# Optimization experiments

Measured on AMD Instinct MI355X. Metric: run time of the kernel, lower is better.

The kernel has to match this reference:

```python
import jax, jax.numpy as jnp
import numpy as np

B, L, E, H = 8, 4096, 1024, 16
D = E // H


def setup_inputs() -> dict:
    key = jax.random.key(0)
    ks = jax.random.split(key, 9)
    s = 1.0 / np.sqrt(E)
    inp = {"x": jax.random.normal(ks[0], (B, L, E), dtype=jnp.float32)}
    names = ["Wq", "bq", "Wk", "bk", "Wv", "bv", "Wo", "bo"]
    for i, n in enumerate(names):
        if n.startswith("W"):
            inp[n] = jax.random.uniform(ks[i + 1], (E, E), dtype=jnp.float32, minval=-s, maxval=s)
        else:
            inp[n] = jax.random.uniform(ks[i + 1], (E,), dtype=jnp.float32, minval=-s, maxval=s)
    return inp


def reference(x, Wq, bq, Wk, bk, Wv, bv, Wo, bo):
    Bb, Ll, _ = x.shape
    # projections: weight is (out, in), y = x @ W^T + b
    Q = jnp.einsum('bli,oi->blo', x, Wq) + bq
    K = jnp.einsum('bli,oi->blo', x, Wk) + bk
    V = jnp.einsum('bli,oi->blo', x, Wv) + bv
    # [B, H, L, D]
    Q = Q.reshape(Bb, Ll, H, D).transpose(0, 2, 1, 3)
    K = K.reshape(Bb, Ll, H, D).transpose(0, 2, 1, 3)
    V = V.reshape(Bb, Ll, H, D).transpose(0, 2, 1, 3)
    # auto-correlation along sequence axis (axis=2)
    q_fft = jnp.fft.rfft(Q, axis=2)
    k_fft = jnp.fft.rfft(K, axis=2)
    corr_time = jnp.fft.irfft(q_fft * jnp.conjugate(k_fft), n=Ll, axis=2)
    corr = jnp.mean(corr_time, axis=-1)              # [B, H, L]
    attn = jax.nn.softmax(corr, axis=-1)             # [B, H, L]
    out = jnp.einsum('bhl,bhld->bhd', attn, V)       # [B, H, D]
    out = out.transpose(0, 2, 1).reshape(Bb, E)      # [B, E] (D-major interleave, as in source)
    out = jnp.einsum('bi,oi->bo', out, Wo) + bo      # [B, E]
    return jnp.repeat(out[:, None, :], Ll, axis=1)   # [B, L, E]
```

## Files before the change

kernel.cpp:

```cpp
#include <hip/hip_runtime.h>
#include <hip/hip_bf16.h>
#include <math.h>

#define B_ 8
#define L_ 4096
#define E_ 1024
#define H_ 16
#define D_ 64

typedef short short8 __attribute__((ext_vector_type(8)));
typedef float f32x4 __attribute__((ext_vector_type(4)));

__device__ __forceinline__ unsigned short f2bf(float f) {
  unsigned int u = __float_as_uint(f);
  unsigned int r = u + 0x7FFFu + ((u >> 16) & 1u);
  return (unsigned short)(r >> 16);
}
__device__ __forceinline__ float bf2f(unsigned short h) {
  return __uint_as_float(((unsigned int)h) << 16);
}

#define GLDS16(g, l)                                                     \
  __builtin_amdgcn_global_load_lds(                                      \
      (const __attribute__((address_space(1))) void*)(g),                \
      (__attribute__((address_space(3))) void*)(l), 16, 0, 0)

__global__ __launch_bounds__(256) void conv_w(
    const float* __restrict__ Wq, const float* __restrict__ Wk,
    const float* __restrict__ Wv, unsigned short* __restrict__ Wb) {
  const int wsel = blockIdx.y;
  const float* W = (wsel == 0) ? Wq : (wsel == 1) ? Wk : Wv;
  size_t i = ((size_t)blockIdx.x * 256 + threadIdx.x) * 4;
  float4 f = *(const float4*)(W + i);
  size_t o = (size_t)wsel * (1024 * 1024) + i;
  *(ushort4*)(Wb + o) =
      make_ushort4(f2bf(f.x), f2bf(f.y), f2bf(f.z), f2bf(f.w));
}

__global__ __launch_bounds__(256) void conv_x(const float* __restrict__ x,
                                              unsigned short* __restrict__ xb) {
  const size_t total = (size_t)B_ * L_ * E_ / 8;
  for (size_t i = (size_t)blockIdx.x * blockDim.x + threadIdx.x; i < total;
       i += (size_t)gridDim.x * blockDim.x) {
    float4 a = ((const float4*)x)[i * 2];
    float4 b = ((const float4*)x)[i * 2 + 1];
    short8 v;
    v[0] = (short)f2bf(a.x); v[1] = (short)f2bf(a.y);
    v[2] = (short)f2bf(a.z); v[3] = (short)f2bf(a.w);
    v[4] = (short)f2bf(b.x); v[5] = (short)f2bf(b.y);
    v[6] = (short)f2bf(b.z); v[7] = (short)f2bf(b.w);
    *(short8*)&xb[i * 8] = v;
  }
}

#define STAGE_A(buf, h, s, t)                                                \
  GLDS16(xb + (size_t)(m0 + (s)*128 + (h)*64 + srow) * E_ + (t)*64 + scol,   \
         &sA[buf][((s)*128 + (h)*64 + wid * 8) * 64])
#define STAGE_B(buf, h, s, t)                                                \
  GLDS16(Wb + (size_t)(n0 + (s)*128 + (h)*32 + brow_i) * E_ + (t)*64 + scol, \
         &sB[buf][((s)*128 + (h)*32 + bw) * 64])

__global__ __launch_bounds__(512) void qkv_gemm8(
    const unsigned short* __restrict__ xb,
    const unsigned short* __restrict__ Wb, const float* __restrict__ bq,
    const float* __restrict__ bk, const float* __restrict__ bv,
    unsigned short* __restrict__ QTb, unsigned short* __restrict__ KTb,
    unsigned short* __restrict__ Vb) {
  __shared__ unsigned short sA[2][256 * 64];
  __shared__ unsigned short sB[2][256 * 64];

  const int tid = threadIdx.x;
  const int wid = tid >> 6, lane = tid & 63;
  const int wr = wid >> 2, wc = wid & 3;
  const int fr = lane & 15, fg = lane >> 4, fr7 = fr & 7;
  const int n0 = blockIdx.x * 256;
  const int m0 = blockIdx.y * 256;

  const int srow = tid >> 3;
  const int scol = ((tid & 7) ^ (srow & 7)) * 8;
  const int brow_i = ((srow >> 5) << 6) + (srow & 31);
  const int bw = ((wid >> 2) << 6) + ((wid & 3) << 3);

  f32x4 acc[8][4];
#pragma unroll
  for (int i = 0; i < 8; ++i)
#pragma unroll
    for (int j = 0; j < 4; ++j) acc[i][j] = (f32x4){0.f, 0.f, 0.f, 0.f};

  STAGE_A(0, 0, 0, 0); STAGE_A(0, 0, 1, 0);
  STAGE_A(0, 1, 0, 0); STAGE_A(0, 1, 1, 0);
  STAGE_B(0, 0, 0, 0); STAGE_B(0, 0, 1, 0);
  STAGE_B(0, 1, 0, 0); STAGE_B(0, 1, 1, 0);
  STAGE_A(1, 0, 0, 1); STAGE_A(1, 0, 1, 1);
  STAGE_B(1, 0, 0, 1); STAGE_B(1, 0, 1, 1);

  const int NT = E_ / 64;
  for (int u = 0; u < NT; ++u) {
    const int cur = u & 1, nxt = cur ^ 1;
    __builtin_amdgcn_sched_barrier(0);
    if (u == NT - 1)
      asm volatile("s_waitcnt vmcnt(0)" ::: "memory");
    else
      asm volatile("s_waitcnt vmcnt(4)" ::: "memory");
    __builtin_amdgcn_sched_barrier(0);
    __builtin_amdgcn_s_barrier();

    short8 af[4][2], b0[2][2], b1[2][2];
#pragma unroll
    for (int i = 0; i < 4; ++i)
#pragma unroll
      for (int kk = 0; kk < 2; ++kk) {
        const int blk = (((kk * 4 + fg) ^ fr7) << 3);
        af[i][kk] = *(const short8*)
            &sA[cur][(wr * 128 + i * 16 + fr) * 64 + blk];
      }
#pragma unroll
    for (int j = 0; j < 2; ++j)
#pragma unroll
      for (int kk = 0; kk < 2; ++kk) {
        const int blk = (((kk * 4 + fg) ^ fr7) << 3);
        b0[j][kk] = *(const short8*)
            &sB[cur][(wc * 64 + j * 16 + fr) * 64 + blk];
        b1[j][kk] = *(const short8*)
            &sB[cur][(wc * 64 + (2 + j) * 16 + fr) * 64 + blk];
      }
    if (u + 1 < NT) {
      STAGE_A(nxt, 1, 0, u + 1); STAGE_A(nxt, 1, 1, u + 1);
      STAGE_B(nxt, 1, 0, u + 1); STAGE_B(nxt, 1, 1, u + 1);
    }
    asm volatile("s_waitcnt lgkmcnt(0)" ::: "memory");
    __builtin_amdgcn_sched_barrier(0);
    __builtin_amdgcn_s_setprio(1);
#pragma unroll
    for (int i = 0; i < 4; ++i)
#pragma unroll
      for (int kk = 0; kk < 2; ++kk) {
        acc[i][0] = __builtin_amdgcn_mfma_f32_16x16x32_bf16(af[i][kk], b0[0][kk], acc[i][0], 0, 0, 0);
        acc[i][1] = __builtin_amdgcn_mfma_f32_16x16x32_bf16(af[i][kk], b0[1][kk], acc[i][1], 0, 0, 0);
        acc[i][2] = __builtin_amdgcn_mfma_f32_16x16x32_bf16(af[i][kk], b1[0][kk], acc[i][2], 0, 0, 0);
        acc[i][3] = __builtin_amdgcn_mfma_f32_16x16x32_bf16(af[i][kk], b1[1][kk], acc[i][3], 0, 0, 0);
      }
    __builtin_amdgcn_s_setprio(0);
    __builtin_amdgcn_s_barrier();

#pragma unroll
    for (int i = 0; i < 4; ++i)
#pragma unroll
      for (int kk = 0; kk < 2; ++kk) {
        const int blk = (((kk * 4 + fg) ^ fr7) << 3);
        af[i][kk] = *(const short8*)
            &sA[cur][(wr * 128 + 64 + i * 16 + fr) * 64 + blk];
      }
    if (u + 2 < NT) {
      STAGE_A(cur, 0, 0, u + 2); STAGE_A(cur, 0, 1, u + 2);
      STAGE_B(cur, 0, 0, u + 2); STAGE_B(cur, 0, 1, u + 2);
    }
    asm volatile("s_waitcnt lgkmcnt(0)" ::: "memory");
    __builtin_amdgcn_sched_barrier(0);
    __builtin_amdgcn_s_setprio(1);
#pragma unroll
    for (int i = 0; i < 4; ++i)
#pragma unroll
      for (int kk = 0; kk < 2; ++kk) {
        acc[4 + i][0] = __builtin_amdgcn_mfma_f32_16x16x32_bf16(af[i][kk], b0[0][kk], acc[4 + i][0], 0, 0, 0);
        acc[4 + i][1] = __builtin_amdgcn_mfma_f32_16x16x32_bf16(af[i][kk], b0[1][kk], acc[4 + i][1], 0, 0, 0);
        acc[4 + i][2] = __builtin_amdgcn_mfma_f32_16x16x32_bf16(af[i][kk], b1[0][kk], acc[4 + i][2], 0, 0, 0);
        acc[4 + i][3] = __builtin_amdgcn_mfma_f32_16x16x32_bf16(af[i][kk], b1[1][kk], acc[4 + i][3], 0, 0, 0);
      }
    __builtin_amdgcn_s_setprio(0);
  }

  const int wsel = n0 >> 10;
  const float* bias = (wsel == 0) ? bq : (wsel == 1) ? bk : bv;
  float br[4];
#pragma unroll
  for (int j = 0; j < 4; ++j)
    br[j] = bias[(n0 & 1023) + wc * 64 + j * 16 + fr];

  if (wsel < 2) {
    unsigned short* T = (wsel == 0) ? QTb : KTb;
    const int b = m0 >> 12;
    const int lbase = (m0 & 4095) + wr * 128 + (fg << 2);
#pragma unroll
    for (int i = 0; i < 8; ++i)
#pragma unroll
      for (int j = 0; j < 4; ++j) {
        const int n_in = (n0 & 1023) + wc * 64 + j * 16 + fr;
        ushort4 v = make_ushort4(f2bf(acc[i][j][0] + br[j]),
                                 f2bf(acc[i][j][1] + br[j]),
                                 f2bf(acc[i][j][2] + br[j]),
                                 f2bf(acc[i][j][3] + br[j]));
        *(ushort4*)&T[((size_t)(b << 10) + n_in) * L_ + lbase + i * 16] = v;
      }
  } else {
#pragma unroll
    for (int i = 0; i < 8; ++i)
#pragma unroll
      for (int j = 0; j < 4; ++j) {
        const int n_in = (n0 & 1023) + wc * 64 + j * 16 + fr;
#pragma unroll
        for (int r = 0; r < 4; ++r) {
          const int m = m0 + wr * 128 + i * 16 + (fg << 2) + r;
          Vb[(size_t)m * E_ + n_in] = f2bf(acc[i][j][r] + br[j]);
        }
      }
  }
}

__device__ __forceinline__ float2 cmulf(float2 a, float2 b) {
  return make_float2(a.x * b.x - a.y * b.y, a.x * b.y + a.y * b.x);
}

__device__ __forceinline__ float2 herm(float2 Zf, float2 Zc) {
  float ax = Zc.x, ay = -Zc.y;
  float qx = 0.5f * (Zf.x + ax), qy = 0.5f * (Zf.y + ay);
  float ux = Zf.x - ax, uy = Zf.y - ay;
  float kx = 0.5f * uy, ky = -0.5f * ux;
  return make_float2(qx * kx + qy * ky, qy * kx - qx * ky);
}

__global__ __launch_bounds__(512) void corr_fft(
    const unsigned short* __restrict__ QTb,
    const unsigned short* __restrict__ KTb, float2* __restrict__ Spart) {
  __shared__ float2 bufA[L_];
  __shared__ float2 bufB[L_];

  const int bh = blockIdx.x, ds = blockIdx.y;
  const int b = bh >> 4, h = bh & (H_ - 1);
  const int tid = threadIdx.x;
  const float sign = -1.0f;

  float2 tw[6], tw5b;
  {
    const float TWO_PI = 6.28318530717958647692f;
#pragma unroll
    for (int st = 0; st < 6; ++st) {
      const int Ns = 1 << (2 * st);
      const int r = tid & (Ns - 1);
      float ang = sign * TWO_PI * (float)r / (float)(4 * Ns);
      __sincosf(ang, &tw[st].y, &tw[st].x);
    }
    const int r5 = (tid + 512) & 1023;
    float ang = sign * TWO_PI * (float)r5 / 4096.f;
    __sincosf(ang, &tw5b.y, &tw5b.x);
  }

  float2 s[4];
#pragma unroll
  for (int q = 0; q < 4; ++q) s[q] = make_float2(0.f, 0.f);

  const size_t baseQK = (size_t)(b * E_ + h * D_) * L_;

  for (int dd = 0; dd < 8; ++dd) {
    const int d = ds * 8 + dd;
    __syncthreads();
    const unsigned short* qp = QTb + baseQK + (size_t)d * L_;
    const unsigned short* kp = KTb + baseQK + (size_t)d * L_;
    {
      ushort4 qa = *(const ushort4*)(qp + tid * 8);
      ushort4 qb = *(const ushort4*)(qp + tid * 8 + 4);
      ushort4 ka = *(const ushort4*)(kp + tid * 8);
      ushort4 kb = *(const ushort4*)(kp + tid * 8 + 4);
      bufA[tid * 8 + 0] = make_float2(bf2f(qa.x), bf2f(ka.x));
      bufA[tid * 8 + 1] = make_float2(bf2f(qa.y), bf2f(ka.y));
      bufA[tid * 8 + 2] = make_float2(bf2f(qa.z), bf2f(ka.z));
      bufA[tid * 8 + 3] = make_float2(bf2f(qa.w), bf2f(ka.w));
      bufA[tid * 8 + 4] = make_float2(bf2f(qb.x), bf2f(kb.x));
      bufA[tid * 8 + 5] = make_float2(bf2f(qb.y), bf2f(kb.y));
      bufA[tid * 8 + 6] = make_float2(bf2f(qb.z), bf2f(kb.z));
      bufA[tid * 8 + 7] = make_float2(bf2f(qb.w), bf2f(kb.w));
    }
    float2* cur = bufA;
    float2* nxt = bufB;
#pragma unroll
    for (int st = 0; st < 6; ++st) {
      const int Ns = 1 << (2 * st);
      __syncthreads();
#pragma unroll
      for (int h2 = 0; h2 < 2; ++h2) {
        const int j = tid + h2 * 512;
        float2 v0 = cur[j];
        float2 v1 = cur[j + 1024];
        float2 v2 = cur[j + 2048];
        float2 v3 = cur[j + 3072];
        const int r = j & (Ns - 1);
        if (st > 0) {
          float2 w1 = (st == 5 && h2 == 1) ? tw5b : tw[st];
          float2 w2 = cmulf(w1, w1);
          float2 w3 = cmulf(w2, w1);
          v1 = cmulf(v1, w1);
          v2 = cmulf(v2, w2);
          v3 = cmulf(v3, w3);
        }
        float2 t0 = make_float2(v0.x + v2.x, v0.y + v2.y);
        float2 t1 = make_float2(v0.x - v2.x, v0.y - v2.y);
        float2 t2 = make_float2(v1.x + v3.x, v1.y + v3.y);
        float2 t3 = make_float2(v1.x - v3.x, v1.y - v3.y);
        float2 t3i = make_float2(-sign * t3.y, sign * t3.x);
        const int idxD = ((j - r) << 2) + r;
        nxt[idxD]          = make_float2(t0.x + t2.x, t0.y + t2.y);
        nxt[idxD + Ns]     = make_float2(t1.x + t3i.x, t1.y + t3i.y);
        nxt[idxD + 2 * Ns] = make_float2(t0.x - t2.x, t0.y - t2.y);
        nxt[idxD + 3 * Ns] = make_float2(t1.x - t3i.x, t1.y - t3i.y);
      }
      float2* tmp = cur; cur = nxt; nxt = tmp;
    }
    __syncthreads();
#pragma unroll
    for (int q = 0; q < 4; ++q) {
      const int f = tid + q * 512;
      float2 Zf = bufA[f];
      float2 Zc = bufA[(L_ - f) & (L_ - 1)];
      float2 r = herm(Zf, Zc);
      s[q].x += r.x;
      s[q].y += r.y;
    }
    if (tid == 0) {
      float2 Zf = bufA[2048];
      float2 r = herm(Zf, Zf);
      s[0].y += r.x;
    }
  }
  float2* out = Spart + (size_t)(bh * 8 + ds) * (L_ / 2);
#pragma unroll
  for (int q = 0; q < 4; ++q) out[tid + q * 512] = s[q];
}

__device__ __forceinline__ void fft_tw_init(float2* tw, int tid, float sign) {
  const float TWO_PI = 6.28318530717958647692f;
#pragma unroll
  for (int st = 0; st < 6; ++st) {
    const int Ns = 1 << (2 * st);
    const int r = tid & (Ns - 1);
    float ang = sign * TWO_PI * (float)r / (float)(4 * Ns);
    __sincosf(ang, &tw[st].y, &tw[st].x);
  }
}

__device__ __forceinline__ void fft4096_tw(float2* __restrict__ A,
                                           float2* __restrict__ Bb, int tid,
                                           float sign,
                                           const float2* __restrict__ tw) {
  float2* cur = A;
  float2* nxt = Bb;
#pragma unroll
  for (int st = 0; st < 6; ++st) {
    const int Ns = 1 << (2 * st);
    __syncthreads();
    const int j = tid;
    float2 v0 = cur[j];
    float2 v1 = cur[j + 1024];
    float2 v2 = cur[j + 2048];
    float2 v3 = cur[j + 3072];
    const int r = j & (Ns - 1);
    if (st > 0) {
      float2 w1 = tw[st];
      float2 w2 = cmulf(w1, w1);
      float2 w3 = cmulf(w2, w1);
      v1 = cmulf(v1, w1);
      v2 = cmulf(v2, w2);
      v3 = cmulf(v3, w3);
    }
    float2 t0 = make_float2(v0.x + v2.x, v0.y + v2.y);
    float2 t1 = make_float2(v0.x - v2.x, v0.y - v2.y);
    float2 t2 = make_float2(v1.x + v3.x, v1.y + v3.y);
    float2 t3 = make_float2(v1.x - v3.x, v1.y - v3.y);
    float2 t3i = make_float2(-sign * t3.y, sign * t3.x);
    const int idxD = ((j - r) << 2) + r;
    nxt[idxD]          = make_float2(t0.x + t2.x, t0.y + t2.y);
    nxt[idxD + Ns]     = make_float2(t1.x + t3i.x, t1.y + t3i.y);
    nxt[idxD + 2 * Ns] = make_float2(t0.x - t2.x, t0.y - t2.y);
    nxt[idxD + 3 * Ns] = make_float2(t1.x - t3i.x, t1.y - t3i.y);
    float2* tmp = cur; cur = nxt; nxt = tmp;
  }
  __syncthreads();
}

__global__ __launch_bounds__(1024) void corr_post(
    const float2* __restrict__ Spart, float* __restrict__ attnW) {
  __shared__ float2 bufA[L_];
  __shared__ float2 bufB[L_];
  __shared__ float red[1024];

  const int bh = blockIdx.x;
  const int tid = threadIdx.x;

  float2 tw[6];
  fft_tw_init(tw, tid, 1.0f);

  const float2* sp = Spart + (size_t)(bh * 8) * (L_ / 2);
  for (int f = tid; f < L_ / 2; f += 1024) {
    float2 s = make_float2(0.f, 0.f);
#pragma unroll
    for (int ds = 0; ds < 8; ++ds) {
      float2 p = sp[(size_t)ds * (L_ / 2) + f];
      s.x += p.x;
      s.y += p.y;
    }
    if (f == 0) {
      bufA[0] = make_float2(s.x, 0.f);
      bufA[L_ / 2] = make_float2(s.y, 0.f);
    } else {
      bufA[f] = s;
      bufA[L_ - f] = make_float2(s.x, -s.y);
    }
  }
  fft4096_tw(bufA, bufB, tid, 1.0f, tw);

  const float cscale = 1.0f / ((float)L_ * (float)D_);
  float lmax = -3.0e38f;
#pragma unroll
  for (int q = 0; q < 4; ++q) lmax = fmaxf(lmax, bufA[tid + q * 1024].x);
  red[tid] = lmax;
  __syncthreads();
  for (int s = 512; s > 0; s >>= 1) {
    if (tid < s) red[tid] = fmaxf(red[tid], red[tid + s]);
    __syncthreads();
  }
  const float gmax = red[0] * cscale;
  __syncthreads();
  float lsum = 0.f;
  float w4[4];
#pragma unroll
  for (int q = 0; q < 4; ++q) {
    w4[q] = __expf(bufA[tid + q * 1024].x * cscale - gmax);
    lsum += w4[q];
  }
  red[tid] = lsum;
  __syncthreads();
  for (int s = 512; s > 0; s >>= 1) {
    if (tid < s) red[tid] += red[tid + s];
    __syncthreads();
  }
  const float inv = 1.0f / red[0];
  float* aw = attnW + (size_t)bh * L_;
#pragma unroll
  for (int q = 0; q < 4; ++q) aw[tid + q * 1024] = w4[q] * inv;
}

__global__ __launch_bounds__(256) void attn_v(
    const float* __restrict__ attnW, const unsigned short* __restrict__ Vb,
    float* __restrict__ out_flat) {
  __shared__ float red[256];
  const int bh = blockIdx.x, dg = blockIdx.y;
  const int b = bh >> 4, h = bh & (H_ - 1);
  const int td = threadIdx.x & 7, tg = threadIdx.x >> 3;

  const float* aw = attnW + (size_t)bh * L_;
  const unsigned short* vb =
      Vb + (size_t)b * L_ * E_ + h * D_ + dg * 8 + td;
  float acc = 0.f;
  for (int l = tg; l < L_; l += 32)
    acc = fmaf(aw[l], bf2f(vb[(size_t)l * E_]), acc);
  red[tg * 8 + td] = acc;
  __syncthreads();
  for (int s = 16; s > 0; s >>= 1) {
    if (tg < s) red[tg * 8 + td] += red[(tg + s) * 8 + td];
    __syncthreads();
  }
  if (tg == 0)
    out_flat[b * E_ + (dg * 8 + td) * H_ + h] = red[td];
}

__global__ __launch_bounds__(256) void final_proj(
    const float* __restrict__ flat, const float* __restrict__ Wo,
    const float* __restrict__ bo, float* __restrict__ y) {
  __shared__ float sf[E_];
  const int b = blockIdx.y;
  const int o0 = blockIdx.x * 64;
  for (int j = threadIdx.x; j < E_; j += 256) sf[j] = flat[b * E_ + j];
  __syncthreads();
  const int oo = threadIdx.x >> 2, part = threadIdx.x & 3;
  const int o = o0 + oo;
  const float4* wr = (const float4*)(Wo + (size_t)o * E_) + part * 64;
  const float4* fr = (const float4*)sf + part * 64;
  float s = 0.f;
#pragma unroll 8
  for (int i = 0; i < 64; ++i) {
    float4 w = wr[i];
    float4 f = fr[i];
    s += w.x * f.x + w.y * f.y + w.z * f.z + w.w * f.w;
  }
  s += __shfl_xor(s, 1);
  s += __shfl_xor(s, 2);
  if (part == 0) y[b * E_ + o] = s + bo[o];
}

__global__ void broadcast_out(const float* __restrict__ y,
                              float4* __restrict__ out4) {
  const size_t total = (size_t)B_ * L_ * (E_ / 4);
  const float4* y4 = (const float4*)y;
  for (size_t i = (size_t)blockIdx.x * blockDim.x + threadIdx.x; i < total;
       i += (size_t)gridDim.x * blockDim.x) {
    size_t e4 = i & (E_ / 4 - 1);
    size_t b = i >> 20;
    out4[i] = y4[b * (E_ / 4) + e4];
  }
}

extern "C" void kernel_launch(void* const* d_in, const int* in_sizes, int n_in,
                              void* d_out, int out_size, void* d_ws,
                              size_t ws_size, hipStream_t stream) {
  const float* x  = (const float*)d_in[0];
  const float* Wq = (const float*)d_in[1];
  const float* bq = (const float*)d_in[2];
  const float* Wk = (const float*)d_in[3];
  const float* bk = (const float*)d_in[4];
  const float* Wv = (const float*)d_in[5];
  const float* bv = (const float*)d_in[6];
  const float* Wo = (const float*)d_in[7];
  const float* bo = (const float*)d_in[8];

  char* w = (char*)d_ws;
  unsigned short* KTb  = (unsigned short*)w;
  unsigned short* Vb   = (unsigned short*)(w + 67108864);
  unsigned short* Wb   = (unsigned short*)(w + 134217728);
  float2* Spart        = (float2*)(w + 140509184);
  float* flat          = (float*)(w + 157286400);
  float* y             = (float*)(w + 157319168);
  float* attnW         = (float*)(w + 157351936);
  unsigned short* QTb  = (unsigned short*)d_out;
  unsigned short* xb   = (unsigned short*)((char*)d_out + 67108864);

  conv_w<<<dim3(1024, 3), 256, 0, stream>>>(Wq, Wk, Wv, Wb);
  conv_x<<<dim3(2048), 256, 0, stream>>>(x, xb);
  qkv_gemm8<<<dim3(12, 128), 512, 0, stream>>>(xb, Wb, bq, bk, bv, QTb, KTb,
                                               Vb);
  corr_fft<<<dim3(B_ * H_, 8), 512, 0, stream>>>(QTb, KTb, Spart);
  corr_post<<<dim3(B_ * H_), 1024, 0, stream>>>(Spart, attnW);
  attn_v<<<dim3(B_ * H_, 8), 256, 0, stream>>>(attnW, Vb, flat);
  final_proj<<<dim3(16, B_), 256, 0, stream>>>(flat, Wo, bo, y);
  broadcast_out<<<dim3(2048), 256, 0, stream>>>(y, (float4*)d_out);
}
```

Before: 466.9 us.

## Switch corr FFT to radix-8 Stockham with XOR-swizzled shared memory

Result: faster. 433.3 us (-7.2%).

```diff
diff --git a/kernel.cpp b/kernel.cpp
--- a/kernel.cpp
+++ b/kernel.cpp
@@ -210,6 +210,22 @@
 __device__ __forceinline__ float2 cmulf(float2 a, float2 b) {
   return make_float2(a.x * b.x - a.y * b.y, a.x * b.y + a.y * b.x);
 }
+__device__ __forceinline__ float2 twc(float2 v, float c, float s, float sign) {
+  return make_float2(v.x * c - v.y * s * sign, v.x * s * sign + v.y * c);
+}
+__device__ __forceinline__ void dft4(float2& a, float2& b, float2& c,
+                                     float2& d, float sign) {
+  float2 t0 = make_float2(a.x + c.x, a.y + c.y);
+  float2 t1 = make_float2(a.x - c.x, a.y - c.y);
+  float2 t2 = make_float2(b.x + d.x, b.y + d.y);
+  float2 t3 = make_float2(b.x - d.x, b.y - d.y);
+  float2 t3i = make_float2(-sign * t3.y, sign * t3.x);
+  a = make_float2(t0.x + t2.x, t0.y + t2.y);
+  b = make_float2(t1.x + t3i.x, t1.y + t3i.y);
+  c = make_float2(t0.x - t2.x, t0.y - t2.y);
+  d = make_float2(t1.x - t3i.x, t1.y - t3i.y);
+}
+#define C45 0.707106781186548f
 
 __device__ __forceinline__ float2 herm(float2 Zf, float2 Zc) {
   float ax = Zc.x, ay = -Zc.y;
@@ -219,6 +235,8 @@
   return make_float2(qx * kx + qy * ky, qy * kx - qx * ky);
 }
 
+__device__ __forceinline__ int swz(int i) { return i ^ ((i >> 4) & 15); }
+
 __global__ __launch_bounds__(512) void corr_fft(
     const unsigned short* __restrict__ QTb,
     const unsigned short* __restrict__ KTb, float2* __restrict__ Spart) {
@@ -230,19 +248,16 @@
   const int tid = threadIdx.x;
   const float sign = -1.0f;
 
-  float2 tw[6], tw5b;
+  float2 twb[4];
   {
     const float TWO_PI = 6.28318530717958647692f;
 #pragma unroll
-    for (int st = 0; st < 6; ++st) {
-      const int Ns = 1 << (2 * st);
+    for (int st = 1; st < 4; ++st) {
+      const int Ns = 1 << (3 * st);
       const int r = tid & (Ns - 1);
-      float ang = sign * TWO_PI * (float)r / (float)(4 * Ns);
-      __sincosf(ang, &tw[st].y, &tw[st].x);
-    }
-    const int r5 = (tid + 512) & 1023;
-    float ang = sign * TWO_PI * (float)r5 / 4096.f;
-    __sincosf(ang, &tw5b.y, &tw5b.x);
+      float ang = sign * TWO_PI * (float)r / (float)(8 * Ns);
+      __sincosf(ang, &twb[st].y, &twb[st].x);
+    }
   }
 
   float2 s[4];
@@ -261,62 +276,74 @@
       ushort4 qb = *(const ushort4*)(qp + tid * 8 + 4);
       ushort4 ka = *(const ushort4*)(kp + tid * 8);
       ushort4 kb = *(const ushort4*)(kp + tid * 8 + 4);
-      bufA[tid * 8 + 0] = make_float2(bf2f(qa.x), bf2f(ka.x));
-      bufA[tid * 8 + 1] = make_float2(bf2f(qa.y), bf2f(ka.y));
-      bufA[tid * 8 + 2] = make_float2(bf2f(qa.z), bf2f(ka.z));
-      bufA[tid * 8 + 3] = make_float2(bf2f(qa.w), bf2f(ka.w));
-      bufA[tid * 8 + 4] = make_float2(bf2f(qb.x), bf2f(kb.x));
-      bufA[tid * 8 + 5] = make_float2(bf2f(qb.y), bf2f(kb.y));
-      bufA[tid * 8 + 6] = make_float2(bf2f(qb.z), bf2f(kb.z));
-      bufA[tid * 8 + 7] = make_float2(bf2f(qb.w), bf2f(kb.w));
+      const int i0 = tid * 8;
+      const int c = (i0 >> 4) & 15;
+      bufA[(i0 + 0) ^ c] = make_float2(bf2f(qa.x), bf2f(ka.x));
+      bufA[(i0 + 1) ^ c] = make_float2(bf2f(qa.y), bf2f(ka.y));
+      bufA[(i0 + 2) ^ c] = make_float2(bf2f(qa.z), bf2f(ka.z));
+      bufA[(i0 + 3) ^ c] = make_float2(bf2f(qa.w), bf2f(ka.w));
+      bufA[(i0 + 4) ^ c] = make_float2(bf2f(qb.x), bf2f(kb.x));
+      bufA[(i0 + 5) ^ c] = make_float2(bf2f(qb.y), bf2f(kb.y));
+      bufA[(i0 + 6) ^ c] = make_float2(bf2f(qb.z), bf2f(kb.z));
+      bufA[(i0 + 7) ^ c] = make_float2(bf2f(qb.w), bf2f(kb.w));
     }
     float2* cur = bufA;
     float2* nxt = bufB;
 #pragma unroll
-    for (int st = 0; st < 6; ++st) {
-      const int Ns = 1 << (2 * st);
+    for (int st = 0; st < 4; ++st) {
+      const int Ns = 1 << (3 * st);
       __syncthreads();
-#pragma unroll
-      for (int h2 = 0; h2 < 2; ++h2) {
-        const int j = tid + h2 * 512;
-        float2 v0 = cur[j];
-        float2 v1 = cur[j + 1024];
-        float2 v2 = cur[j + 2048];
-        float2 v3 = cur[j + 3072];
-        const int r = j & (Ns - 1);
-        if (st > 0) {
-          float2 w1 = (st == 5 && h2 == 1) ? tw5b : tw[st];
-          float2 w2 = cmulf(w1, w1);
-          float2 w3 = cmulf(w2, w1);
-          v1 = cmulf(v1, w1);
-          v2 = cmulf(v2, w2);
-          v3 = cmulf(v3, w3);
-        }
-        float2 t0 = make_float2(v0.x + v2.x, v0.y + v2.y);
-        float2 t1 = make_float2(v0.x - v2.x, v0.y - v2.y);
-        float2 t2 = make_float2(v1.x + v3.x, v1.y + v3.y);
-        float2 t3 = make_float2(v1.x - v3.x, v1.y - v3.y);
-        float2 t3i = make_float2(-sign * t3.y, sign * t3.x);
-        const int idxD = ((j - r) << 2) + r;
-        nxt[idxD]          = make_float2(t0.x + t2.x, t0.y + t2.y);
-        nxt[idxD + Ns]     = make_float2(t1.x + t3i.x, t1.y + t3i.y);
-        nxt[idxD + 2 * Ns] = make_float2(t0.x - t2.x, t0.y - t2.y);
-        nxt[idxD + 3 * Ns] = make_float2(t1.x - t3i.x, t1.y - t3i.y);
-      }
+      const int j = tid;
+      float2 v[8];
+#pragma unroll
+      for (int m = 0; m < 8; ++m) v[m] = cur[swz(j + (m << 9))];
+      const int r = j & (Ns - 1);
+      if (st > 0) {
+        float2 w1 = twb[st];
+        float2 w2 = cmulf(w1, w1);
+        float2 w3 = cmulf(w2, w1);
+        float2 w4 = cmulf(w2, w2);
+        float2 w5 = cmulf(w4, w1);
+        float2 w6 = cmulf(w4, w2);
+        float2 w7 = cmulf(w4, w3);
+        v[1] = cmulf(v[1], w1);
+        v[2] = cmulf(v[2], w2);
+        v[3] = cmulf(v[3], w3);
+        v[4] = cmulf(v[4], w4);
+        v[5] = cmulf(v[5], w5);
+        v[6] = cmulf(v[6], w6);
+        v[7] = cmulf(v[7], w7);
+      }
+      float2 e0 = v[0], e1 = v[2], e2 = v[4], e3 = v[6];
+      float2 o0 = v[1], o1 = v[3], o2 = v[5], o3 = v[7];
+      dft4(e0, e1, e2, e3, sign);
+      dft4(o0, o1, o2, o3, sign);
+      o1 = twc(o1, C45, C45, sign);
+      o2 = twc(o2, 0.0f, 1.0f, sign);
+      o3 = twc(o3, -C45, C45, sign);
+      const int idxD = ((j - r) << 3) + r;
+      nxt[swz(idxD)]          = make_float2(e0.x + o0.x, e0.y + o0.y);
+      nxt[swz(idxD + Ns)]     = make_float2(e1.x + o1.x, e1.y + o1.y);
+      nxt[swz(idxD + 2 * Ns)] = make_float2(e2.x + o2.x, e2.y + o2.y);
+      nxt[swz(idxD + 3 * Ns)] = make_float2(e3.x + o3.x, e3.y + o3.y);
+      nxt[swz(idxD + 4 * Ns)] = make_float2(e0.x - o0.x, e0.y - o0.y);
+      nxt[swz(idxD + 5 * Ns)] = make_float2(e1.x - o1.x, e1.y - o1.y);
+      nxt[swz(idxD + 6 * Ns)] = make_float2(e2.x - o2.x, e2.y - o2.y);
+      nxt[swz(idxD + 7 * Ns)] = make_float2(e3.x - o3.x, e3.y - o3.y);
       float2* tmp = cur; cur = nxt; nxt = tmp;
     }
     __syncthreads();
 #pragma unroll
     for (int q = 0; q < 4; ++q) {
       const int f = tid + q * 512;
-      float2 Zf = bufA[f];
-      float2 Zc = bufA[(L_ - f) & (L_ - 1)];
+      float2 Zf = bufA[swz(f)];
+      float2 Zc = bufA[swz((L_ - f) & (L_ - 1))];
       float2 r = herm(Zf, Zc);
       s[q].x += r.x;
       s[q].y += r.y;
     }
     if (tid == 0) {
-      float2 Zf = bufA[2048];
+      float2 Zf = bufA[swz(2048)];
       float2 r = herm(Zf, Zf);
       s[0].y += r.x;
     }
```
